# Optimization experiments

Measured on AMD Instinct MI355X. Metric: run time of the kernel, lower is better.

Reference implementation:

```python
import jax, jax.numpy as jnp
import numpy as np
import math


def get_alibi_slopes(n_heads: int) -> np.ndarray:
    # Bloom-style ALiBi slopes.
    cp2 = 2 ** math.floor(math.log2(n_heads))
    base = 2.0 ** (-(2.0 ** -(math.log2(cp2) - 3)))
    slopes = base ** np.arange(1, cp2 + 1, dtype=np.float32)
    if cp2 != n_heads:
        extra_base = 2.0 ** (-(2.0 ** -(math.log2(2 * cp2) - 3)))
        extra = extra_base ** np.arange(1, 2 * (n_heads - cp2) + 1, 2, dtype=np.float32)
        slopes = np.concatenate([slopes, extra])
    return slopes.astype(np.float32)


def setup_inputs() -> dict:
    key = jax.random.key(0)
    k1, k2, k3 = jax.random.split(key, 3)
    B, S, D, H = 2, 2048, 2048, 16
    T = B * S
    return {
        "hidden_states": jax.random.normal(k1, (T, D), dtype=jnp.float32) * 0.02,
        "qkv_weight": jax.random.normal(k2, (3, D, D), dtype=jnp.float32) * 0.02,
        "o_proj_weight": jax.random.normal(k3, (D, D), dtype=jnp.float32) * 0.02,
        "batch": B,
        "seq_len": S,
        "n_heads": H,
    }


def reference(hidden_states, qkv_weight, o_proj_weight, batch, seq_len, n_heads):
    T, D = hidden_states.shape
    head_dim = D // n_heads
    sm_scale = 1.0 / math.sqrt(head_dim)
    slopes = jnp.asarray(get_alibi_slopes(n_heads))  # [H]

    # QKV projection: equivalent of bmm(hidden.expand(3,-1,-1), qkv_weight)
    qkv = jnp.einsum("td,cde->cte", hidden_states, qkv_weight)  # [3, T, D]
    q, k, v = qkv.reshape(3, batch, seq_len, n_heads, head_dim)

    # Varlen causal attention with ALiBi (prefill / context phase).
    scores = jnp.einsum("bqhd,bkhd->bhqk", q, k) * sm_scale  # [B,H,S,S]
    pos = jnp.arange(seq_len)
    rel = (pos[None, :] - pos[:, None]).astype(jnp.float32)  # k_idx - q_idx
    scores = scores + slopes[None, :, None, None] * rel[None, None]
    causal = pos[None, :] <= pos[:, None]  # [S,S]
    scores = jnp.where(causal[None, None], scores, jnp.finfo(scores.dtype).min)
    probs = jax.nn.softmax(scores, axis=-1)
    attn = jnp.einsum("bhqk,bkhd->bqhd", probs, v)  # [B,S,H,Dh]

    attn = attn.reshape(T, D)
    return attn @ o_proj_weight
```

## Files before the change

kernel.cpp:

```cpp
#include <hip/hip_runtime.h>
#include <math.h>
#include <stdint.h>

typedef __bf16 bf16x8_t __attribute__((ext_vector_type(8)));
typedef float  f32x4_t  __attribute__((ext_vector_type(4)));
typedef unsigned short u16;


__device__ __forceinline__ u16 f2bf(float f) {
  unsigned u = __float_as_uint(f);
  u += 0x7FFFu + ((u >> 16) & 1u);
  return (u16)(u >> 16);
}

__device__ __forceinline__ void gload_lds16(const u16* gsrc, u16* ldst) {
  __builtin_amdgcn_global_load_lds(
      (__attribute__((address_space(1))) void*)(const_cast<u16*>(gsrc)),
      (__attribute__((address_space(3))) void*)(ldst),
      16, 0, 0);
}

__device__ __forceinline__ int sw8(int row, int e) { return e ^ ((row & 7) << 3); }

__device__ __forceinline__ void store_out(float* C, long idx, float v) { C[idx] = v; }
__device__ __forceinline__ void store_out(u16* C, long idx, float v) { C[idx] = f2bf(v); }

__device__ __forceinline__ float alibi_slope(int h, int H) {
  int cp2 = 1, lg = 0;
  while (cp2 * 2 <= H) { cp2 *= 2; lg++; }
  if (h < cp2) {
    double e = exp2((double)-(lg - 3));
    return (float)exp2(-e * (double)(h + 1));
  } else {
    double e = exp2((double)-(lg + 1 - 3));
    return (float)exp2(-e * (double)(2 * (h - cp2) + 1));
  }
}

#define FENCE() asm volatile("" ::: "memory")
#define BARRIER() do { FENCE(); __builtin_amdgcn_s_barrier(); \
                       __builtin_amdgcn_sched_barrier(0); FENCE(); } while (0)
#define WAITLGKM() do { asm volatile("s_waitcnt lgkmcnt(0)" ::: "memory"); \
                        __builtin_amdgcn_sched_barrier(0); } while (0)


__global__ __launch_bounds__(256) void k_cast_bf16(const float* __restrict__ in,
                                                   u16* __restrict__ out, long n) {
  long i = ((long)blockIdx.x * 256 + threadIdx.x) * 4;
  if (i + 3 < n) {
    float4 v = *reinterpret_cast<const float4*>(in + i);
    ushort4 o;
    o.x = f2bf(v.x); o.y = f2bf(v.y); o.z = f2bf(v.z); o.w = f2bf(v.w);
    *reinterpret_cast<ushort4*>(out + i) = o;
  }
}


__global__ __launch_bounds__(256) void k_transpose_cast(const float* __restrict__ in,
                                                        u16* __restrict__ out,
                                                        int R, int C) {
  __shared__ float tile[32][33];
  const float* inz = in + (long)blockIdx.z * R * C;
  u16* outz = out + (long)blockIdx.z * R * C;
  const int tx = threadIdx.x & 31, ty = threadIdx.x >> 5;
  const int r0 = blockIdx.y * 32, c0 = blockIdx.x * 32;
#pragma unroll
  for (int i = 0; i < 4; ++i)
    tile[ty + i * 8][tx] = inz[(long)(r0 + ty + i * 8) * C + c0 + tx];
  __syncthreads();
#pragma unroll
  for (int i = 0; i < 4; ++i)
    outz[(long)(c0 + ty + i * 8) * R + r0 + tx] = f2bf(tile[tx][ty + i * 8]);
}


__global__ __launch_bounds__(256) void k_transpose_v(const u16* __restrict__ V,
                                                     u16* __restrict__ Vt,
                                                     int S, int D, int Dh, int H) {
  __shared__ u16 tile[32][33];
  const int bh = blockIdx.z, b = bh / H, h = bh % H;
  const int tx = threadIdx.x & 31, ty = threadIdx.x >> 5;
  const int s0 = blockIdx.x * 32, d0 = blockIdx.y * 32;
  const u16* vin = V + (long)b * S * D + (long)h * Dh;
#pragma unroll
  for (int i = 0; i < 4; ++i)
    tile[ty + i * 8][tx] = vin[(long)(s0 + ty + i * 8) * D + d0 + tx];
  __syncthreads();
  u16* vout = Vt + (long)bh * Dh * S;
#pragma unroll
  for (int i = 0; i < 4; ++i)
    vout[(long)(d0 + ty + i * 8) * S + s0 + tx] = tile[tx][ty + i * 8];
}


__device__ __forceinline__ void stage16(const u16* __restrict__ g, long grow0, int K,
                                        int kt, int lr0, u16 (*lds)[64], int lane) {
  const int e = (lane & 7) * 8;
#pragma unroll
  for (int i = 0; i < 2; ++i) {
    const int r = lr0 + i * 8 + (lane >> 3);
    gload_lds16(g + (grow0 + r) * (long)K + kt + (e ^ ((r & 7) << 3)), &lds[lr0 + i * 8][0]);
  }
}

template <typename OUT_T>
__global__ __launch_bounds__(512, 2) void k_gemm8(const u16* __restrict__ A,
                                                  const u16* __restrict__ Bt,
                                                  OUT_T* __restrict__ Cb,
                                                  int M, int N, int K, long matStride) {
  __shared__ u16 As[2][256][64];
  __shared__ u16 Bs[2][256][64];

  const int tid = threadIdx.x, wid = tid >> 6, lane = tid & 63;
  const int wr = wid >> 2, wc = wid & 3;
  const int frow = lane & 15, fk8 = (lane >> 4) * 8;
  const int orow = (lane >> 4) * 4, ocol = lane & 15;

  const int nwg = gridDim.x * gridDim.y;
  const int orig = blockIdx.y * gridDim.x + blockIdx.x;
  const int q = nwg >> 3, rr = nwg & 7;
  const int xcd = orig & 7, sl = orig >> 3;
  const int wg = (xcd < rr ? xcd * (q + 1) : rr * (q + 1) + (xcd - rr) * q) + sl;
  const int by = wg / gridDim.x, bx = wg % gridDim.x;

  const long abase = (long)by * 256, bbase = (long)bx * 256;

  const int bg0 = (wid >> 1) * 64 + (wid & 1) * 16;
  const int ag0 = (wid >> 2) * 128 + (wid & 3) * 16;

  f32x4_t acc[8][4];
#pragma unroll
  for (int m = 0; m < 8; ++m)
#pragma unroll
    for (int n = 0; n < 4; ++n)
#pragma unroll
      for (int r = 0; r < 4; ++r) acc[m][n][r] = 0.f;

  const int nt = K >> 6;

  stage16(Bt, bbase, K, 0, bg0, Bs[0], lane);
  stage16(Bt, bbase, K, 0, bg0 + 32, Bs[0], lane);
  stage16(A, abase, K, 0, ag0, As[0], lane);
  stage16(A, abase, K, 0, ag0 + 64, As[0], lane);
  asm volatile("s_waitcnt vmcnt(2)" ::: "memory");
  BARRIER();

  bf16x8_t afr[4][2], bfr[4][2];
  int cur = 0;

  for (int t = 0; t < nt; ++t) {
    const int ktn = (t + 1) << 6;
    const bool hn = (t + 1 < nt);
    const int nb = cur ^ 1;

#pragma unroll
    for (int m = 0; m < 4; ++m) {
      const int r = wr * 128 + m * 16 + frow;
      afr[m][0] = *reinterpret_cast<const bf16x8_t*>(&As[cur][r][sw8(r, fk8)]);
      afr[m][1] = *reinterpret_cast<const bf16x8_t*>(&As[cur][r][sw8(r, 32 + fk8)]);
    }
#pragma unroll
    for (int n = 0; n < 2; ++n) {
      const int r = wc * 64 + n * 16 + frow;
      bfr[n][0] = *reinterpret_cast<const bf16x8_t*>(&Bs[cur][r][sw8(r, fk8)]);
      bfr[n][1] = *reinterpret_cast<const bf16x8_t*>(&Bs[cur][r][sw8(r, 32 + fk8)]);
    }
    if (hn) stage16(Bt, bbase, K, ktn, bg0, Bs[nb], lane);
    BARRIER();
    WAITLGKM();
    __builtin_amdgcn_s_setprio(1);
#pragma unroll
    for (int m = 0; m < 4; ++m)
#pragma unroll
      for (int n = 0; n < 2; ++n) {
        acc[m][n] = __builtin_amdgcn_mfma_f32_16x16x32_bf16(afr[m][0], bfr[n][0], acc[m][n], 0, 0, 0);
        acc[m][n] = __builtin_amdgcn_mfma_f32_16x16x32_bf16(afr[m][1], bfr[n][1], acc[m][n], 0, 0, 0);
      }
    __builtin_amdgcn_s_setprio(0);
    BARRIER();

#pragma unroll
    for (int n = 0; n < 2; ++n) {
      const int r = wc * 64 + 32 + n * 16 + frow;
      bfr[2 + n][0] = *reinterpret_cast<const bf16x8_t*>(&Bs[cur][r][sw8(r, fk8)]);
      bfr[2 + n][1] = *reinterpret_cast<const bf16x8_t*>(&Bs[cur][r][sw8(r, 32 + fk8)]);
    }
    if (hn) stage16(Bt, bbase, K, ktn, bg0 + 32, Bs[nb], lane);
    BARRIER();
    WAITLGKM();
    __builtin_amdgcn_s_setprio(1);
#pragma unroll
    for (int m = 0; m < 4; ++m)
#pragma unroll
      for (int n = 0; n < 2; ++n) {
        acc[m][2 + n] = __builtin_amdgcn_mfma_f32_16x16x32_bf16(afr[m][0], bfr[2 + n][0], acc[m][2 + n], 0, 0, 0);
        acc[m][2 + n] = __builtin_amdgcn_mfma_f32_16x16x32_bf16(afr[m][1], bfr[2 + n][1], acc[m][2 + n], 0, 0, 0);
      }
    __builtin_amdgcn_s_setprio(0);
    if (hn) asm volatile("s_waitcnt vmcnt(4)" ::: "memory");
    else    asm volatile("s_waitcnt vmcnt(0)" ::: "memory");
    BARRIER();

#pragma unroll
    for (int m = 0; m < 4; ++m) {
      const int r = wr * 128 + 64 + m * 16 + frow;
      afr[m][0] = *reinterpret_cast<const bf16x8_t*>(&As[cur][r][sw8(r, fk8)]);
      afr[m][1] = *reinterpret_cast<const bf16x8_t*>(&As[cur][r][sw8(r, 32 + fk8)]);
    }
    if (hn) stage16(A, abase, K, ktn, ag0, As[nb], lane);
    BARRIER();
    WAITLGKM();
    __builtin_amdgcn_s_setprio(1);
#pragma unroll
    for (int m = 0; m < 4; ++m)
#pragma unroll
      for (int n = 0; n < 2; ++n) {
        acc[4 + m][n] = __builtin_amdgcn_mfma_f32_16x16x32_bf16(afr[m][0], bfr[n][0], acc[4 + m][n], 0, 0, 0);
        acc[4 + m][n] = __builtin_amdgcn_mfma_f32_16x16x32_bf16(afr[m][1], bfr[n][1], acc[4 + m][n], 0, 0, 0);
      }
    __builtin_amdgcn_s_setprio(0);
    BARRIER();

    if (hn) stage16(A, abase, K, ktn, ag0 + 64, As[nb], lane);
    __builtin_amdgcn_s_setprio(1);
#pragma unroll
    for (int m = 0; m < 4; ++m)
#pragma unroll
      for (int n = 0; n < 2; ++n) {
        acc[4 + m][2 + n] = __builtin_amdgcn_mfma_f32_16x16x32_bf16(afr[m][0], bfr[2 + n][0], acc[4 + m][2 + n], 0, 0, 0);
        acc[4 + m][2 + n] = __builtin_amdgcn_mfma_f32_16x16x32_bf16(afr[m][1], bfr[2 + n][1], acc[4 + m][2 + n], 0, 0, 0);
      }
    __builtin_amdgcn_s_setprio(0);
    if (hn) asm volatile("s_waitcnt vmcnt(2)" ::: "memory");
    BARRIER();

    cur ^= 1;
  }

#pragma unroll
  for (int m = 0; m < 8; ++m)
#pragma unroll
    for (int n = 0; n < 4; ++n)
#pragma unroll
      for (int r = 0; r < 4; ++r) {
        const long row = abase + wr * 128 + m * 16 + orow + r;
        const int col = (int)bbase + wc * 64 + n * 16 + ocol;
        const long idx = (long)(col >> 11) * matStride + row * 2048 + (col & 2047);
        store_out(Cb, idx, acc[m][n][r]);
      }
}


__global__ __launch_bounds__(256) void k_attn(const u16* __restrict__ Q,
                                              const u16* __restrict__ Kb,
                                              const u16* __restrict__ Vt,
                                              u16* __restrict__ Out,
                                              int B, int S, int H, int D, float sm_scale) {
  __shared__ u16 Ks[64][128];
  __shared__ u16 Vs[128][64];
  __shared__ u16 Ps[128][64];

  const int tid = threadIdx.x, wid = tid >> 6, lane = tid & 63;

  const int nq = gridDim.x, nbh = gridDim.y;
  const int lin = blockIdx.x + nq * blockIdx.y;
  const int qb0 = lin / nbh;
  const int bh  = lin % nbh;
  const int qb  = (qb0 < nq / 2) ? qb0 : (nq + nq / 2 - 1 - qb0);

  const int b = bh / H, h = bh % H;
  const int Dh = D / H;

  const float slope = alibi_slope(h, H);
  const long qrow0 = (long)b * S + qb * 128 + wid * 32;

  const int frow = lane & 15;
  const int fk8  = (lane >> 4) * 8;
  const int orow = (lane >> 4) * 4;
  const int ocol = lane & 15;

  bf16x8_t aq[2][4];
#pragma unroll
  for (int m = 0; m < 2; ++m)
#pragma unroll
    for (int kk = 0; kk < 4; ++kk)
      aq[m][kk] = *reinterpret_cast<const bf16x8_t*>(
          Q + (qrow0 + m * 16 + frow) * (long)D + h * Dh + kk * 32 + fk8);

  f32x4_t oacc[2][8];
#pragma unroll
  for (int m = 0; m < 2; ++m)
#pragma unroll
    for (int no = 0; no < 8; ++no)
#pragma unroll
      for (int r = 0; r < 4; ++r) oacc[m][no][r] = 0.f;

  float mrun[2][4], lrun[2][4];
#pragma unroll
  for (int m = 0; m < 2; ++m)
#pragma unroll
    for (int r = 0; r < 4; ++r) { mrun[m][r] = -3.0e38f; lrun[m][r] = 0.f; }

  const int qg0 = qb * 128 + wid * 32;
  const int ktiles = 2 * qb + 2;

  for (int kt = 0; kt < ktiles; ++kt) {
    __syncthreads();
#pragma unroll
    for (int i = 0; i < 4; ++i) {
      const int lr = i * 16 + wid * 4;
      const int r  = lr + (lane >> 4);
      gload_lds16(Kb + ((long)b * S + kt * 64 + r) * (long)D + h * Dh + sw8(r, (lane & 15) * 8),
                  &Ks[lr][0]);
    }
#pragma unroll
    for (int i = 0; i < 4; ++i) {
      const int lr = i * 32 + wid * 8;
      const int r  = lr + (lane >> 3);
      gload_lds16(Vt + ((long)bh * Dh + r) * (long)S + kt * 64 + sw8(r, (lane & 7) * 8),
                  &Vs[lr][0]);
    }
    __syncthreads();

    const bool active = (kt * 64) <= (qg0 + 31);

    if (active) {
      f32x4_t sacc[2][4];
#pragma unroll
      for (int m = 0; m < 2; ++m)
#pragma unroll
        for (int n = 0; n < 4; ++n)
#pragma unroll
          for (int r = 0; r < 4; ++r) sacc[m][n][r] = 0.f;

#pragma unroll
      for (int kk = 0; kk < 4; ++kk) {
        bf16x8_t bk[4];
#pragma unroll
        for (int n = 0; n < 4; ++n) {
          const int krow = n * 16 + frow;
          bk[n] = *reinterpret_cast<const bf16x8_t*>(&Ks[krow][sw8(krow, kk * 32 + fk8)]);
        }
#pragma unroll
        for (int m = 0; m < 2; ++m)
#pragma unroll
          for (int n = 0; n < 4; ++n)
            sacc[m][n] = __builtin_amdgcn_mfma_f32_16x16x32_bf16(aq[m][kk], bk[n], sacc[m][n], 0, 0, 0);
      }

      float tmax[2][4];
#pragma unroll
      for (int m = 0; m < 2; ++m)
#pragma unroll
        for (int r = 0; r < 4; ++r) tmax[m][r] = -3.0e38f;

#pragma unroll
      for (int m = 0; m < 2; ++m)
#pragma unroll
        for (int n = 0; n < 4; ++n)
#pragma unroll
          for (int r = 0; r < 4; ++r) {
            const int qg = qg0 + m * 16 + orow + r;
            const int kg = kt * 64 + n * 16 + ocol;
            float v = sacc[m][n][r] * sm_scale + slope * (float)(kg - qg);
            v = (kg <= qg) ? v : -1.0e30f;
            sacc[m][n][r] = v;
            tmax[m][r] = fmaxf(tmax[m][r], v);
          }
#pragma unroll
      for (int m = 0; m < 2; ++m)
#pragma unroll
        for (int r = 0; r < 4; ++r) {
          float t = tmax[m][r];
          t = fmaxf(t, __shfl_xor(t, 1));
          t = fmaxf(t, __shfl_xor(t, 2));
          t = fmaxf(t, __shfl_xor(t, 4));
          t = fmaxf(t, __shfl_xor(t, 8));
          tmax[m][r] = t;
        }

      float tsum[2][4];
#pragma unroll
      for (int m = 0; m < 2; ++m)
#pragma unroll
        for (int r = 0; r < 4; ++r) {
          const float mnew = fmaxf(mrun[m][r], tmax[m][r]);
          const float alpha = __expf(mrun[m][r] - mnew);
          mrun[m][r] = mnew;
          lrun[m][r] *= alpha;
#pragma unroll
          for (int no = 0; no < 8; ++no) oacc[m][no][r] *= alpha;
          tsum[m][r] = 0.f;
        }
#pragma unroll
      for (int m = 0; m < 2; ++m)
#pragma unroll
        for (int n = 0; n < 4; ++n)
#pragma unroll
          for (int r = 0; r < 4; ++r) {
            const float p = __expf(sacc[m][n][r] - mrun[m][r]);
            tsum[m][r] += p;
            const int prow = wid * 32 + m * 16 + orow + r;
            Ps[prow][sw8(prow, n * 16 + ocol)] = f2bf(p);
          }
#pragma unroll
      for (int m = 0; m < 2; ++m)
#pragma unroll
        for (int r = 0; r < 4; ++r) {
          float t = tsum[m][r];
          t += __shfl_xor(t, 1);
          t += __shfl_xor(t, 2);
          t += __shfl_xor(t, 4);
          t += __shfl_xor(t, 8);
          lrun[m][r] += t;
        }
    }

    __syncthreads();

    if (active) {
#pragma unroll
      for (int kk = 0; kk < 2; ++kk) {
        bf16x8_t pa[2];
        const int prow0 = wid * 32 + frow;
        const int prow1 = wid * 32 + 16 + frow;
        pa[0] = *reinterpret_cast<const bf16x8_t*>(&Ps[prow0][sw8(prow0, kk * 32 + fk8)]);
        pa[1] = *reinterpret_cast<const bf16x8_t*>(&Ps[prow1][sw8(prow1, kk * 32 + fk8)]);
#pragma unroll
        for (int no = 0; no < 8; ++no) {
          const int vrow = no * 16 + frow;
          bf16x8_t bv = *reinterpret_cast<const bf16x8_t*>(&Vs[vrow][sw8(vrow, kk * 32 + fk8)]);
          oacc[0][no] = __builtin_amdgcn_mfma_f32_16x16x32_bf16(pa[0], bv, oacc[0][no], 0, 0, 0);
          oacc[1][no] = __builtin_amdgcn_mfma_f32_16x16x32_bf16(pa[1], bv, oacc[1][no], 0, 0, 0);
        }
      }
    }
  }

#pragma unroll
  for (int m = 0; m < 2; ++m)
#pragma unroll
    for (int r = 0; r < 4; ++r) {
      const float rl = 1.0f / lrun[m][r];
      const long trow = qrow0 + m * 16 + orow + r;
#pragma unroll
      for (int no = 0; no < 8; ++no)
        Out[trow * (long)D + h * Dh + no * 16 + ocol] = f2bf(oacc[m][no][r] * rl);
    }
}


extern "C" void kernel_launch(void* const* d_in, const int* in_sizes, int n_in,
                              void* d_out, int out_size, void* d_ws, size_t ws_size,
                              hipStream_t stream) {
  const float* hs   = (const float*)d_in[0];
  const float* qkvw = (const float*)d_in[1];
  const float* ow   = (const float*)d_in[2];

  const int D = 2048, B = 2, H = 16;
  const long TD = (long)in_sizes[0];
  const long DD = (long)in_sizes[2];
  const int T = (int)(TD / D);
  const int S = T / B;
  const int Dh = D / H;
  const float sm_scale = 1.0f / sqrtf((float)Dh);

  u16* ws  = (u16*)d_ws;
  u16* hsb = ws;
  u16* wt  = ws + TD;
  u16* owt = wt + 3 * DD;
  u16* qkv = owt + DD;
  u16* vt   = wt;
  u16* attn = hsb;

  k_cast_bf16<<<dim3((unsigned)(TD / 1024)), 256, 0, stream>>>(hs, hsb, TD);
  k_transpose_cast<<<dim3(D / 32, D / 32, 3), 256, 0, stream>>>(qkvw, wt, D, D);
  k_transpose_cast<<<dim3(D / 32, D / 32, 1), 256, 0, stream>>>(ow, owt, D, D);
  k_gemm8<u16><<<dim3((3 * D) / 256, T / 256), 512, 0, stream>>>(
      hsb, wt, qkv, T, 3 * D, D, TD);
  k_transpose_v<<<dim3(S / 32, Dh / 32, B * H), 256, 0, stream>>>(
      qkv + 2 * TD, vt, S, D, Dh, H);
  k_attn<<<dim3(S / 128, B * H), 256, 0, stream>>>(
      qkv, qkv + TD, vt, attn, B, S, H, D, sm_scale);
  k_gemm8<float><<<dim3(D / 256, T / 256), 512, 0, stream>>>(
      attn, owt, (float*)d_out, T, D, D, 0L);
}
```

Baseline: 332.8 us.

## Fold softmax scale into Q projection and shrink attention query tile to 64

The QKV GEMM epilogue now multiplies the Q columns by sm_scale*log2e, so the attention kernel can use exp2 directly. ALiBi bias becomes a per-column constant added to the scores, and causal masking is applied only on the diagonal tile. The attention query block drops from 128 to 64 rows, with one 16-row MFMA group per wave. This doubles the grid and removes the wasted inactive-wave iterations in the causal loop. The cost is more K/V tile reloads across blocks and less MFMA work per LDS load.

```diff
diff --git a/kernel.cpp b/kernel.cpp
--- a/kernel.cpp
+++ b/kernel.cpp
@@ -107,7 +107,8 @@
 __global__ __launch_bounds__(512, 2) void k_gemm8(const u16* __restrict__ A,
                                                   const u16* __restrict__ Bt,
                                                   OUT_T* __restrict__ Cb,
-                                                  int M, int N, int K, long matStride) {
+                                                  int M, int N, int K, long matStride,
+                                                  float qs) {
   __shared__ u16 As[2][256][64];
   __shared__ u16 Bs[2][256][64];
 
@@ -245,8 +246,9 @@
       for (int r = 0; r < 4; ++r) {
         const long row = abase + wr * 128 + m * 16 + orow + r;
         const int col = (int)bbase + wc * 64 + n * 16 + ocol;
+        const float sc = ((col >> 11) == 0) ? qs : 1.0f;
         const long idx = (long)(col >> 11) * matStride + row * 2048 + (col & 2047);
-        store_out(Cb, idx, acc[m][n][r]);
+        store_out(Cb, idx, acc[m][n][r] * sc);
       }
 }
 
@@ -255,10 +257,11 @@
                                               const u16* __restrict__ Kb,
                                               const u16* __restrict__ Vt,
                                               u16* __restrict__ Out,
-                                              int B, int S, int H, int D, float sm_scale) {
+                                              int B, int S, int H, int D,
+                                              float log2e) {
   __shared__ u16 Ks[64][128];
   __shared__ u16 Vs[128][64];
-  __shared__ u16 Ps[128][64];
+  __shared__ u16 Ps[64][64];
 
   const int tid = threadIdx.x, wid = tid >> 6, lane = tid & 63;
 
@@ -271,182 +274,168 @@
   const int b = bh / H, h = bh % H;
   const int Dh = D / H;
 
-  const float slope = alibi_slope(h, H);
-  const long qrow0 = (long)b * S + qb * 128 + wid * 32;
+  const float slope2 = alibi_slope(h, H) * log2e;
+  const long qrow0 = (long)b * S + qb * 64 + wid * 16;
 
   const int frow = lane & 15;
   const int fk8  = (lane >> 4) * 8;
   const int orow = (lane >> 4) * 4;
   const int ocol = lane & 15;
 
-  bf16x8_t aq[2][4];
-#pragma unroll
-  for (int m = 0; m < 2; ++m)
-#pragma unroll
-    for (int kk = 0; kk < 4; ++kk)
-      aq[m][kk] = *reinterpret_cast<const bf16x8_t*>(
-          Q + (qrow0 + m * 16 + frow) * (long)D + h * Dh + kk * 32 + fk8);
-
-  f32x4_t oacc[2][8];
-#pragma unroll
-  for (int m = 0; m < 2; ++m)
-#pragma unroll
-    for (int no = 0; no < 8; ++no)
-#pragma unroll
-      for (int r = 0; r < 4; ++r) oacc[m][no][r] = 0.f;
-
-  float mrun[2][4], lrun[2][4];
-#pragma unroll
-  for (int m = 0; m < 2; ++m)
-#pragma unroll
-    for (int r = 0; r < 4; ++r) { mrun[m][r] = -3.0e38f; lrun[m][r] = 0.f; }
-
-  const int qg0 = qb * 128 + wid * 32;
-  const int ktiles = 2 * qb + 2;
-
-  for (int kt = 0; kt < ktiles; ++kt) {
+  bf16x8_t aq[4];
+#pragma unroll
+  for (int kk = 0; kk < 4; ++kk)
+    aq[kk] = *reinterpret_cast<const bf16x8_t*>(
+        Q + (qrow0 + frow) * (long)D + h * Dh + kk * 32 + fk8);
+
+  float cw[4];
+#pragma unroll
+  for (int n = 0; n < 4; ++n) cw[n] = slope2 * (float)(n * 16 + ocol);
+
+  f32x4_t oacc[8];
+#pragma unroll
+  for (int no = 0; no < 8; ++no)
+#pragma unroll
+    for (int r = 0; r < 4; ++r) oacc[no][r] = 0.f;
+
+  float Mrun[4], lrun[4];
+#pragma unroll
+  for (int r = 0; r < 4; ++r) { Mrun[r] = -3.0e38f; lrun[r] = 0.f; }
+
+  const u16* kbase = Kb + (long)b * S * D + h * Dh;
+  const u16* vbase = Vt + (long)bh * Dh * S;
+
+  const int ntile = qb + 1;
+
+  for (int kt = 0; kt < ntile; ++kt) {
     __syncthreads();
 #pragma unroll
     for (int i = 0; i < 4; ++i) {
       const int lr = i * 16 + wid * 4;
       const int r  = lr + (lane >> 4);
-      gload_lds16(Kb + ((long)b * S + kt * 64 + r) * (long)D + h * Dh + sw8(r, (lane & 15) * 8),
-                  &Ks[lr][0]);
+      gload_lds16(kbase + ((long)kt * 64 + r) * (long)D + sw8(r, (lane & 15) * 8), &Ks[lr][0]);
     }
 #pragma unroll
     for (int i = 0; i < 4; ++i) {
       const int lr = i * 32 + wid * 8;
       const int r  = lr + (lane >> 3);
-      gload_lds16(Vt + ((long)bh * Dh + r) * (long)S + kt * 64 + sw8(r, (lane & 7) * 8),
-                  &Vs[lr][0]);
+      gload_lds16(vbase + (long)r * S + kt * 64 + sw8(r, (lane & 7) * 8), &Vs[lr][0]);
     }
     __syncthreads();
 
-    const bool active = (kt * 64) <= (qg0 + 31);
-
-    if (active) {
-      f32x4_t sacc[2][4];
-#pragma unroll
-      for (int m = 0; m < 2; ++m)
-#pragma unroll
-        for (int n = 0; n < 4; ++n)
-#pragma unroll
-          for (int r = 0; r < 4; ++r) sacc[m][n][r] = 0.f;
-
-#pragma unroll
-      for (int kk = 0; kk < 4; ++kk) {
-        bf16x8_t bk[4];
-#pragma unroll
-        for (int n = 0; n < 4; ++n) {
-          const int krow = n * 16 + frow;
-          bk[n] = *reinterpret_cast<const bf16x8_t*>(&Ks[krow][sw8(krow, kk * 32 + fk8)]);
+    f32x4_t sacc[4];
+#pragma unroll
+    for (int n = 0; n < 4; ++n)
+#pragma unroll
+      for (int r = 0; r < 4; ++r) sacc[n][r] = 0.f;
+
+#pragma unroll
+    for (int kk = 0; kk < 4; ++kk) {
+      bf16x8_t bk[4];
+#pragma unroll
+      for (int n = 0; n < 4; ++n) {
+        const int krow = n * 16 + frow;
+        bk[n] = *reinterpret_cast<const bf16x8_t*>(&Ks[krow][sw8(krow, kk * 32 + fk8)]);
+      }
+#pragma unroll
+      for (int n = 0; n < 4; ++n)
+        sacc[n] = __builtin_amdgcn_mfma_f32_16x16x32_bf16(aq[kk], bk[n], sacc[n], 0, 0, 0);
+    }
+
+    const float tb = slope2 * (float)(kt << 6);
+    float cbn[4];
+#pragma unroll
+    for (int n = 0; n < 4; ++n) cbn[n] = tb + cw[n];
+
+    float tmax[4];
+#pragma unroll
+    for (int r = 0; r < 4; ++r) tmax[r] = -3.0e38f;
+
+    if (kt == qb) {
+#pragma unroll
+      for (int n = 0; n < 4; ++n)
+#pragma unroll
+        for (int r = 0; r < 4; ++r) {
+          float v = sacc[n][r] + cbn[n];
+          v = (n * 16 + ocol <= wid * 16 + orow + r) ? v : -1.0e30f;
+          sacc[n][r] = v;
+          tmax[r] = fmaxf(tmax[r], v);
         }
-#pragma unroll
-        for (int m = 0; m < 2; ++m)
-#pragma unroll
-          for (int n = 0; n < 4; ++n)
-            sacc[m][n] = __builtin_amdgcn_mfma_f32_16x16x32_bf16(aq[m][kk], bk[n], sacc[m][n], 0, 0, 0);
-      }
-
-      float tmax[2][4];
-#pragma unroll
-      for (int m = 0; m < 2; ++m)
-#pragma unroll
-        for (int r = 0; r < 4; ++r) tmax[m][r] = -3.0e38f;
-
-#pragma unroll
-      for (int m = 0; m < 2; ++m)
-#pragma unroll
-        for (int n = 0; n < 4; ++n)
-#pragma unroll
-          for (int r = 0; r < 4; ++r) {
-            const int qg = qg0 + m * 16 + orow + r;
-            const int kg = kt * 64 + n * 16 + ocol;
-            float v = sacc[m][n][r] * sm_scale + slope * (float)(kg - qg);
-            v = (kg <= qg) ? v : -1.0e30f;
-            sacc[m][n][r] = v;
-            tmax[m][r] = fmaxf(tmax[m][r], v);
-          }
-#pragma unroll
-      for (int m = 0; m < 2; ++m)
+    } else {
+#pragma unroll
+      for (int n = 0; n < 4; ++n)
 #pragma unroll
         for (int r = 0; r < 4; ++r) {
-          float t = tmax[m][r];
-          t = fmaxf(t, __shfl_xor(t, 1));
-          t = fmaxf(t, __shfl_xor(t, 2));
-          t = fmaxf(t, __shfl_xor(t, 4));
-          t = fmaxf(t, __shfl_xor(t, 8));
-          tmax[m][r] = t;
+          const float v = sacc[n][r] + cbn[n];
+          sacc[n][r] = v;
+          tmax[r] = fmaxf(tmax[r], v);
         }
-
-      float tsum[2][4];
-#pragma unroll
-      for (int m = 0; m < 2; ++m)
-#pragma unroll
-        for (int r = 0; r < 4; ++r) {
-          const float mnew = fmaxf(mrun[m][r], tmax[m][r]);
-          const float alpha = __expf(mrun[m][r] - mnew);
-          mrun[m][r] = mnew;
-          lrun[m][r] *= alpha;
-#pragma unroll
-          for (int no = 0; no < 8; ++no) oacc[m][no][r] *= alpha;
-          tsum[m][r] = 0.f;
-        }
-#pragma unroll
-      for (int m = 0; m < 2; ++m)
-#pragma unroll
-        for (int n = 0; n < 4; ++n)
-#pragma unroll
-          for (int r = 0; r < 4; ++r) {
-            const float p = __expf(sacc[m][n][r] - mrun[m][r]);
-            tsum[m][r] += p;
-            const int prow = wid * 32 + m * 16 + orow + r;
-            Ps[prow][sw8(prow, n * 16 + ocol)] = f2bf(p);
-          }
-#pragma unroll
-      for (int m = 0; m < 2; ++m)
-#pragma unroll
-        for (int r = 0; r < 4; ++r) {
-          float t = tsum[m][r];
-          t += __shfl_xor(t, 1);
-          t += __shfl_xor(t, 2);
-          t += __shfl_xor(t, 4);
-          t += __shfl_xor(t, 8);
-          lrun[m][r] += t;
-        }
+    }
+#pragma unroll
+    for (int r = 0; r < 4; ++r) {
+      float t = tmax[r];
+      t = fmaxf(t, __shfl_xor(t, 1));
+      t = fmaxf(t, __shfl_xor(t, 2));
+      t = fmaxf(t, __shfl_xor(t, 4));
+      t = fmaxf(t, __shfl_xor(t, 8));
+      tmax[r] = t;
+    }
+
+#pragma unroll
+    for (int r = 0; r < 4; ++r) {
+      const float mnew = fmaxf(Mrun[r], tmax[r]);
+      const float alpha = exp2f(Mrun[r] - mnew);
+      Mrun[r] = mnew;
+      lrun[r] *= alpha;
+#pragma unroll
+      for (int no = 0; no < 8; ++no) oacc[no][r] *= alpha;
+    }
+
+    float tsum[4];
+#pragma unroll
+    for (int r = 0; r < 4; ++r) tsum[r] = 0.f;
+#pragma unroll
+    for (int n = 0; n < 4; ++n)
+#pragma unroll
+      for (int r = 0; r < 4; ++r) {
+        const float p = exp2f(sacc[n][r] - Mrun[r]);
+        tsum[r] += p;
+        const int prow = wid * 16 + orow + r;
+        Ps[prow][sw8(prow, n * 16 + ocol)] = f2bf(p);
+      }
+#pragma unroll
+    for (int r = 0; r < 4; ++r) {
+      float t = tsum[r];
+      t += __shfl_xor(t, 1);
+      t += __shfl_xor(t, 2);
+      t += __shfl_xor(t, 4);
+      t += __shfl_xor(t, 8);
+      lrun[r] += t;
     }
 
     __syncthreads();
 
-    if (active) {
-#pragma unroll
-      for (int kk = 0; kk < 2; ++kk) {
-        bf16x8_t pa[2];
-        const int prow0 = wid * 32 + frow;
-        const int prow1 = wid * 32 + 16 + frow;
-        pa[0] = *reinterpret_cast<const bf16x8_t*>(&Ps[prow0][sw8(prow0, kk * 32 + fk8)]);
-        pa[1] = *reinterpret_cast<const bf16x8_t*>(&Ps[prow1][sw8(prow1, kk * 32 + fk8)]);
-#pragma unroll
-        for (int no = 0; no < 8; ++no) {
-          const int vrow = no * 16 + frow;
-          bf16x8_t bv = *reinterpret_cast<const bf16x8_t*>(&Vs[vrow][sw8(vrow, kk * 32 + fk8)]);
-          oacc[0][no] = __builtin_amdgcn_mfma_f32_16x16x32_bf16(pa[0], bv, oacc[0][no], 0, 0, 0);
-          oacc[1][no] = __builtin_amdgcn_mfma_f32_16x16x32_bf16(pa[1], bv, oacc[1][no], 0, 0, 0);
-        }
-      }
-    }
-  }
-
-#pragma unroll
-  for (int m = 0; m < 2; ++m)
-#pragma unroll
-    for (int r = 0; r < 4; ++r) {
-      const float rl = 1.0f / lrun[m][r];
-      const long trow = qrow0 + m * 16 + orow + r;
-#pragma unroll
-      for (int no = 0; no < 8; ++no)
-        Out[trow * (long)D + h * Dh + no * 16 + ocol] = f2bf(oacc[m][no][r] * rl);
-    }
+#pragma unroll
+    for (int kk = 0; kk < 2; ++kk) {
+      const int prow = wid * 16 + frow;
+      bf16x8_t pa = *reinterpret_cast<const bf16x8_t*>(&Ps[prow][sw8(prow, kk * 32 + fk8)]);
+#pragma unroll
+      for (int no = 0; no < 8; ++no) {
+        const int vrow = no * 16 + frow;
+        bf16x8_t bv = *reinterpret_cast<const bf16x8_t*>(&Vs[vrow][sw8(vrow, kk * 32 + fk8)]);
+        oacc[no] = __builtin_amdgcn_mfma_f32_16x16x32_bf16(pa, bv, oacc[no], 0, 0, 0);
+      }
+    }
+  }
+
+#pragma unroll
+  for (int r = 0; r < 4; ++r) {
+    const float rl = 1.0f / lrun[r];
+    const long trow = qrow0 + orow + r;
+#pragma unroll
+    for (int no = 0; no < 8; ++no)
+      Out[trow * (long)D + h * Dh + no * 16 + ocol] = f2bf(oacc[no][r] * rl);
+  }
 }
 
 
@@ -463,7 +452,8 @@
   const int T = (int)(TD / D);
   const int S = T / B;
   const int Dh = D / H;
-  const float sm_scale = 1.0f / sqrtf((float)Dh);
+  const float log2e = 1.44269504f;
+  const float qs = (1.0f / sqrtf((float)Dh)) * log2e;
 
   u16* ws  = (u16*)d_ws;
   u16* hsb = ws;
@@ -477,11 +467,11 @@
   k_transpose_cast<<<dim3(D / 32, D / 32, 3), 256, 0, stream>>>(qkvw, wt, D, D);
   k_transpose_cast<<<dim3(D / 32, D / 32, 1), 256, 0, stream>>>(ow, owt, D, D);
   k_gemm8<u16><<<dim3((3 * D) / 256, T / 256), 512, 0, stream>>>(
-      hsb, wt, qkv, T, 3 * D, D, TD);
+      hsb, wt, qkv, T, 3 * D, D, TD, qs);
   k_transpose_v<<<dim3(S / 32, Dh / 32, B * H), 256, 0, stream>>>(
       qkv + 2 * TD, vt, S, D, Dh, H);
-  k_attn<<<dim3(S / 128, B * H), 256, 0, stream>>>(
-      qkv, qkv + TD, vt, attn, B, S, H, D, sm_scale);
+  k_attn<<<dim3(S / 64, B * H), 256, 0, stream>>>(
+      qkv, qkv + TD, vt, attn, B, S, H, D, log2e);
   k_gemm8<float><<<dim3(D / 256, T / 256), 512, 0, stream>>>(
-      attn, owt, (float*)d_out, T, D, D, 0L);
-}
+      attn, owt, (float*)d_out, T, D, D, 0L, 1.0f);
+}
```

New measurement: 312.2 us. -6.2%, faster.
